# Performance work log

Measured on AMD Instinct MI355X. Metric: run time of the kernel, lower is better.

## Reference

```python
import jax, jax.numpy as jnp
import numpy as np
import math

B, S, D = 4, 4096, 2048
H = 16
DH = D // H  # 128
EPS = 1e-5


def _layer_norm(x, g, b):
    m = jnp.mean(x, axis=-1, keepdims=True)
    v = jnp.mean(jnp.square(x - m), axis=-1, keepdims=True)
    return (x - m) * jax.lax.rsqrt(v + EPS) * g + b


def setup_inputs() -> dict:
    key = jax.random.key(0)
    ks = jax.random.split(key, 12)
    s = 0.02
    return {
        "X": jax.random.normal(ks[0], (B, S, D), dtype=jnp.float32),
        "Wq": jax.random.normal(ks[1], (D, D), dtype=jnp.float32) * s,
        "bq": jnp.zeros((D,), dtype=jnp.float32),
        "Wk": jax.random.normal(ks[2], (D, D), dtype=jnp.float32) * s,
        "bk": jnp.zeros((D,), dtype=jnp.float32),
        "Wv": jax.random.normal(ks[3], (D, D), dtype=jnp.float32) * s,
        "bv": jnp.zeros((D,), dtype=jnp.float32),
        "g1": jnp.ones((D,), dtype=jnp.float32),
        "beta1": jnp.zeros((D,), dtype=jnp.float32),
        "W1": jax.random.normal(ks[4], (D, D), dtype=jnp.float32) * s,
        "b1": jnp.zeros((D,), dtype=jnp.float32),
        "W2": jax.random.normal(ks[5], (D, D), dtype=jnp.float32) * s,
        "b2": jnp.zeros((D,), dtype=jnp.float32),
        "g2": jnp.ones((D,), dtype=jnp.float32),
        "beta2": jnp.zeros((D,), dtype=jnp.float32),
    }


def reference(X, Wq, bq, Wk, bk, Wv, bv, g1, beta1, W1, b1, W2, b2, g2, beta2):
    # --- MultiHeadSelfAttention (faithful: .view, so attention is over HEADS per token) ---
    q = (X @ Wq + bq).reshape(B, S, H, DH)
    k = (X @ Wk + bk).reshape(B, S, H, DH)
    v = (X @ Wv + bv).reshape(B, S, H, DH)
    # [B, S, H, H] scores: heads attend to heads within the same position
    att = jnp.einsum('bshd,bstd->bsht', q, k) / math.sqrt(DH)
    att = jax.nn.softmax(att, axis=-1)
    y = jnp.einsum('bsht,bstd->bshd', att, v).reshape(B, S, D)
    # --- residual + LN1 ---
    X1 = _layer_norm(X + y, g1, beta1)
    # --- FeedForward: D -> D -> D with exact GELU ---
    h = jax.nn.gelu(X1 @ W1 + b1, approximate=False)
    y2 = h @ W2 + b2
    # --- residual + LN2 ---
    return _layer_norm(X1 + y2, g2, beta2)
```

## Files before the change

### kernel.cpp

```cpp
#include <hip/hip_runtime.h>
#include <math.h>

#define DM 2048
#define NT 16384
#define KD 2048

typedef __bf16 bf16x8 __attribute__((ext_vector_type(8)));
typedef float  f32x4  __attribute__((ext_vector_type(4)));

__device__ __forceinline__ void gld_lds16(const void* g, void* l) {
  __builtin_amdgcn_global_load_lds(
      (const __attribute__((address_space(1))) unsigned int*)g,
      (__attribute__((address_space(3))) unsigned int*)l, 16, 0, 0);
}

__global__ __launch_bounds__(256) void k_cast(const float* __restrict__ x,
                                              __bf16* __restrict__ y) {
  const size_t i = ((size_t)blockIdx.x * 256 + threadIdx.x) * 8;
  const float4 a = *(const float4*)(x + i);
  const float4 b = *(const float4*)(x + i + 4);
  bf16x8 o;
  o[0]=(__bf16)a.x; o[1]=(__bf16)a.y; o[2]=(__bf16)a.z; o[3]=(__bf16)a.w;
  o[4]=(__bf16)b.x; o[5]=(__bf16)b.y; o[6]=(__bf16)b.z; o[7]=(__bf16)b.w;
  *(bf16x8*)(y + i) = o;
}

__global__ __launch_bounds__(256) void k_transpose(const float* __restrict__ W,
                                                   __bf16* __restrict__ Wt) {
  __shared__ float t[32][33];
  const int tx = threadIdx.x, ty = threadIdx.y;
  const int n  = blockIdx.x * 32 + tx;
  const int k0 = blockIdx.y * 32;
  #pragma unroll
  for (int j = 0; j < 32; j += 8) t[ty + j][tx] = W[(size_t)(k0 + ty + j) * DM + n];
  __syncthreads();
  const int kk = k0 + tx;
  const int n0 = blockIdx.x * 32;
  #pragma unroll
  for (int j = 0; j < 32; j += 8)
    Wt[(size_t)(n0 + ty + j) * KD + kk] = (__bf16)t[tx][ty + j];
}

__global__ __launch_bounds__(256) void k_bias3(const float* __restrict__ a,
                                               const float* __restrict__ b,
                                               const float* __restrict__ c,
                                               float* __restrict__ o) {
  const int i = blockIdx.x * 256 + threadIdx.x;
  o[i] = (i < 2048) ? a[i] : ((i < 4096) ? b[i - 2048] : c[i - 4096]);
}

__global__ __launch_bounds__(256, 2) void k_gemm(
    const __bf16* __restrict__ A, const __bf16* __restrict__ Bt,
    const float* __restrict__ bias, const int mode, const int ntile_n,
    const int NS,
    __bf16* __restrict__ outb, const float* __restrict__ resf,
    const __bf16* __restrict__ resb, float* __restrict__ outf) {
  __shared__ __bf16 As[128 * 64];
  __shared__ __bf16 Bs[128 * 64];
  const int tid  = threadIdx.x;
  const int wave = tid >> 6, lane = tid & 63;
  const int quad = lane >> 4, r16 = lane & 15;
  const int bid = blockIdx.x;
  const int m0 = (bid / ntile_n) * 128;
  const int n0 = (bid % ntile_n) * 128;
  const int wm = (wave >> 1) * 64, wn = (wave & 1) * 64;

  const int lrow = lane >> 3;
  const int gblk = (lane & 7) ^ lrow;
  const __bf16* Ap[4];
  const __bf16* Bp[4];
  __bf16* AsW[4];
  __bf16* BsW[4];
  #pragma unroll
  for (int i = 0; i < 4; i++) {
    const int sr = i * 32 + wave * 8 + lrow;
    Ap[i] = A  + (size_t)(m0 + sr) * KD + gblk * 8;
    Bp[i] = Bt + (size_t)(n0 + sr) * KD + gblk * 8;
    AsW[i] = &As[i * 2048 + wave * 512];
    BsW[i] = &Bs[i * 2048 + wave * 512];
  }

  f32x4 acc[4][4] = {};

  for (int k0 = 0; k0 < KD; k0 += 64) {
    #pragma unroll
    for (int i = 0; i < 4; i++) {
      gld_lds16(Ap[i] + k0, AsW[i]);
      gld_lds16(Bp[i] + k0, BsW[i]);
    }
    __syncthreads();
    #pragma unroll
    for (int ks = 0; ks < 2; ks++) {
      const int fb = ((ks * 4 + quad) ^ (r16 & 7)) * 8;
      bf16x8 af[4], bfr[4];
      #pragma unroll
      for (int mi = 0; mi < 4; mi++)
        af[mi] = *(const bf16x8*)&As[(wm + mi * 16 + r16) * 64 + fb];
      #pragma unroll
      for (int ni = 0; ni < 4; ni++)
        bfr[ni] = *(const bf16x8*)&Bs[(wn + ni * 16 + r16) * 64 + fb];
      #pragma unroll
      for (int mi = 0; mi < 4; mi++)
        #pragma unroll
        for (int ni = 0; ni < 4; ni++)
          acc[mi][ni] = __builtin_amdgcn_mfma_f32_16x16x32_bf16(af[mi], bfr[ni], acc[mi][ni], 0, 0, 0);
    }
    __syncthreads();
  }

  if (mode <= 1) {
    __bf16* eb = &As[wave * 2048];
    #pragma unroll
    for (int half = 0; half < 2; half++) {
      #pragma unroll
      for (int nj = 0; nj < 2; nj++) {
        const int ni = half * 2 + nj;
        const int gn = n0 + wn + ni * 16 + r16;
        const float bv = bias[gn];
        #pragma unroll
        for (int mi = 0; mi < 4; mi++) {
          #pragma unroll
          for (int r = 0; r < 4; r++) {
            float v = acc[mi][ni][r] + bv;
            if (mode == 1) v = 0.5f * v * (1.0f + erff(v * 0.70710678118654752f));
            eb[(mi * 16 + quad * 4 + r) * 32 + nj * 16 + r16] = (__bf16)v;
          }
        }
      }
      #pragma unroll
      for (int rd = 0; rd < 4; rd++) {
        const int row = rd * 16 + (lane >> 2);
        const int c0 = (lane & 3) * 8;
        bf16x8 vv = *(const bf16x8*)&eb[row * 32 + c0];
        *(bf16x8*)(outb + (size_t)(m0 + wm + row) * NS + n0 + wn + half * 32 + c0) = vv;
      }
    }
  } else {
    #pragma unroll
    for (int ni = 0; ni < 4; ni++) {
      const int gn = n0 + wn + ni * 16 + r16;
      const float bv = bias[gn];
      #pragma unroll
      for (int mi = 0; mi < 4; mi++) {
        const int gm = m0 + wm + mi * 16 + quad * 4;
        if (mode == 2) {
          #pragma unroll
          for (int r = 0; r < 4; r++) {
            const size_t o = (size_t)(gm + r) * NS + gn;
            outf[o] = acc[mi][ni][r] + bv + resf[o];
          }
        } else {
          #pragma unroll
          for (int r = 0; r < 4; r++) {
            const size_t o = (size_t)(gm + r) * NS + gn;
            outf[o] = acc[mi][ni][r] + bv + (float)resb[o];
          }
        }
      }
    }
  }
}

__global__ __launch_bounds__(256) void k_attn_ln1(
    const __bf16* __restrict__ QKV, const float* __restrict__ X,
    const float* __restrict__ g1, const float* __restrict__ be1,
    float* __restrict__ X1, __bf16* __restrict__ X1b, const int use_f32) {
  __shared__ float qs[16 * 132];
  __shared__ float ks[16 * 132];
  __shared__ float vs[16 * 132];
  __shared__ float p[256];
  __shared__ float red[8];
  const int tid = threadIdx.x;
  const size_t qbase = (size_t)blockIdx.x * 6144;
  const size_t base  = (size_t)blockIdx.x * DM;
  const int e0 = tid * 8;

  {
    const int row = e0 >> 7, c0 = e0 & 127;
    bf16x8 qv = *(const bf16x8*)(QKV + qbase + e0);
    bf16x8 kv = *(const bf16x8*)(QKV + qbase + 2048 + e0);
    bf16x8 vv = *(const bf16x8*)(QKV + qbase + 4096 + e0);
    #pragma unroll
    for (int j = 0; j < 8; j++) {
      qs[row * 132 + c0 + j] = (float)qv[j];
      ks[row * 132 + c0 + j] = (float)kv[j];
      vs[row * 132 + c0 + j] = (float)vv[j];
    }
  }
  __syncthreads();

  {
    const int h = tid >> 4, t = tid & 15;
    const float* qp = &qs[h * 132];
    const float* kp = &ks[t * 132];
    float s = 0.f;
    #pragma unroll
    for (int d = 0; d < 128; d++) s += qp[d] * kp[d];
    s *= 0.08838834764831845f;
    float mx = s;
    #pragma unroll
    for (int off = 8; off; off >>= 1) mx = fmaxf(mx, __shfl_xor(mx, off, 16));
    const float e = expf(s - mx);
    float sum = e;
    #pragma unroll
    for (int off = 8; off; off >>= 1) sum += __shfl_xor(sum, off, 16);
    p[tid] = e / sum;
  }
  __syncthreads();

  float zloc[8];
  float zs = 0.f, zq = 0.f;
  {
    const float4 x1 = *(const float4*)(X + base + e0);
    const float4 x2 = *(const float4*)(X + base + e0 + 4);
    const float xr[8] = {x1.x, x1.y, x1.z, x1.w, x2.x, x2.y, x2.z, x2.w};
    const int hh = e0 >> 7;
    const int d0 = e0 & 127;
    const float* pp = &p[hh * 16];
    #pragma unroll
    for (int j = 0; j < 8; j++) {
      float y = 0.f;
      #pragma unroll
      for (int t2 = 0; t2 < 16; t2++) y += pp[t2] * vs[t2 * 132 + d0 + j];
      const float z = xr[j] + y;
      zloc[j] = z; zs += z; zq += z * z;
    }
  }
  #pragma unroll
  for (int off = 32; off; off >>= 1) {
    zs += __shfl_xor(zs, off, 64);
    zq += __shfl_xor(zq, off, 64);
  }
  const int wave = tid >> 6, lane = tid & 63;
  if (lane == 0) { red[wave] = zs; red[4 + wave] = zq; }
  __syncthreads();
  zs = red[0] + red[1] + red[2] + red[3];
  zq = red[4] + red[5] + red[6] + red[7];
  const float mean = zs * (1.f / DM);
  const float var = zq * (1.f / DM) - mean * mean;
  const float rstd = rsqrtf(var + 1e-5f);
  {
    float o[8];
    #pragma unroll
    for (int j = 0; j < 8; j++)
      o[j] = (zloc[j] - mean) * rstd * g1[e0 + j] + be1[e0 + j];
    if (use_f32) {
      *(float4*)(X1 + base + e0)     = make_float4(o[0], o[1], o[2], o[3]);
      *(float4*)(X1 + base + e0 + 4) = make_float4(o[4], o[5], o[6], o[7]);
    }
    bf16x8 ob;
    #pragma unroll
    for (int j = 0; j < 8; j++) ob[j] = (__bf16)o[j];
    *(bf16x8*)(X1b + base + e0) = ob;
  }
}

__global__ __launch_bounds__(256) void k_ln2(const float* __restrict__ Z,
                                             const float* __restrict__ g,
                                             const float* __restrict__ be,
                                             float* __restrict__ out) {
  __shared__ float red[8];
  const int tid = threadIdx.x;
  const size_t base = (size_t)blockIdx.x * DM;
  const int e0 = tid * 8;
  const float4 a = *(const float4*)(Z + base + e0);
  const float4 b = *(const float4*)(Z + base + e0 + 4);
  float z[8] = {a.x, a.y, a.z, a.w, b.x, b.y, b.z, b.w};
  float zs = 0.f, zq = 0.f;
  #pragma unroll
  for (int j = 0; j < 8; j++) { zs += z[j]; zq += z[j] * z[j]; }
  #pragma unroll
  for (int off = 32; off; off >>= 1) {
    zs += __shfl_xor(zs, off, 64);
    zq += __shfl_xor(zq, off, 64);
  }
  const int wave = tid >> 6, lane = tid & 63;
  if (lane == 0) { red[wave] = zs; red[4 + wave] = zq; }
  __syncthreads();
  zs = red[0] + red[1] + red[2] + red[3];
  zq = red[4] + red[5] + red[6] + red[7];
  const float mean = zs * (1.f / DM);
  const float var = zq * (1.f / DM) - mean * mean;
  const float rstd = rsqrtf(var + 1e-5f);
  float o[8];
  #pragma unroll
  for (int j = 0; j < 8; j++)
    o[j] = (z[j] - mean) * rstd * g[e0 + j] + be[e0 + j];
  *(float4*)(out + base + e0)     = make_float4(o[0], o[1], o[2], o[3]);
  *(float4*)(out + base + e0 + 4) = make_float4(o[4], o[5], o[6], o[7]);
}

extern "C" void kernel_launch(void* const* d_in, const int* in_sizes, int n_in,
                              void* d_out, int out_size, void* d_ws, size_t ws_size,
                              hipStream_t stream) {
  const float* X   = (const float*)d_in[0];
  const float* Wq  = (const float*)d_in[1];
  const float* bq  = (const float*)d_in[2];
  const float* Wk  = (const float*)d_in[3];
  const float* bk  = (const float*)d_in[4];
  const float* Wv  = (const float*)d_in[5];
  const float* bv  = (const float*)d_in[6];
  const float* g1  = (const float*)d_in[7];
  const float* be1 = (const float*)d_in[8];
  const float* W1  = (const float*)d_in[9];
  const float* b1  = (const float*)d_in[10];
  const float* W2  = (const float*)d_in[11];
  const float* b2  = (const float*)d_in[12];
  const float* g2  = (const float*)d_in[13];
  const float* be2 = (const float*)d_in[14];
  float* out = (float*)d_out;

  char* ws = (char*)d_ws;
  size_t off = 0;
  auto alloc = [&](size_t b) -> char* {
    char* p = ws + off;
    off += (b + 255) & ~(size_t)255;
    return p;
  };
  const size_t EL  = (size_t)NT * DM;
  const size_t EL3 = (size_t)NT * 6144;
  __bf16* Xb    = (__bf16*)alloc(EL * 2);
  __bf16* Wqkvt = (__bf16*)alloc((size_t)6144 * KD * 2);
  __bf16* W1t   = (__bf16*)alloc((size_t)DM * KD * 2);
  __bf16* W2t   = (__bf16*)alloc((size_t)DM * KD * 2);
  float*  b3    = (float*)alloc(6144 * 4);
  __bf16* QKVb  = (__bf16*)alloc(EL3 * 2);
  __bf16* X1b   = (__bf16*)alloc(EL * 2);
  const int use_f32 = (ws_size >= off + EL * 4) ? 1 : 0;
  float* X1 = nullptr;
  if (use_f32) X1 = (float*)alloc(EL * 4);
  __bf16* Hb = Xb;
  float*  Z  = (float*)QKVb;

  k_cast<<<dim3(NT * DM / 2048), dim3(256), 0, stream>>>(X, Xb);
  dim3 tb(32, 8), tg(64, 64);
  k_transpose<<<tg, tb, 0, stream>>>(Wq, Wqkvt);
  k_transpose<<<tg, tb, 0, stream>>>(Wk, Wqkvt + (size_t)2048 * KD);
  k_transpose<<<tg, tb, 0, stream>>>(Wv, Wqkvt + (size_t)4096 * KD);
  k_transpose<<<tg, tb, 0, stream>>>(W1, W1t);
  k_transpose<<<tg, tb, 0, stream>>>(W2, W2t);
  k_bias3<<<dim3(24), dim3(256), 0, stream>>>(bq, bk, bv, b3);

  k_gemm<<<dim3((NT / 128) * 48), dim3(256), 0, stream>>>(
      Xb, Wqkvt, b3, 0, 48, 6144, QKVb, nullptr, nullptr, nullptr);
  k_attn_ln1<<<dim3(NT), dim3(256), 0, stream>>>(QKVb, X, g1, be1, X1, X1b, use_f32);
  k_gemm<<<dim3((NT / 128) * 16), dim3(256), 0, stream>>>(
      X1b, W1t, b1, 1, 16, 2048, Hb, nullptr, nullptr, nullptr);
  k_gemm<<<dim3((NT / 128) * 16), dim3(256), 0, stream>>>(
      Hb, W2t, b2, use_f32 ? 2 : 3, 16, 2048, nullptr, X1, X1b, Z);
  k_ln2<<<dim3(NT), dim3(256), 0, stream>>>(Z, g2, be2, out);
}
```

Baseline: 1.240 ms.

## Pipeline GEMM K-loop with 4-stage LDS ring buffer and tile swizzle

Replaces the single-buffered 64-wide K loop, which synchronized twice per step, with a 4-stage ring of 32-wide K slices. Loads are issued three stages ahead using direct global-to-LDS copies, and a partial vmcnt wait with one barrier per step lets memory traffic overlap the MFMA work. It also remaps block IDs in groups of 8 for better L2 locality and raises wave priority around the MFMA block. The cost is 64KB of LDS, which limits occupancy, and the code now assumes KD=2048 with a hardcoded iteration count and no LDS swizzle, so bank conflicts may appear.

After: 1.405 ms. 1.13x slower.

```diff
diff --git a/kernel.cpp b/kernel.cpp
--- a/kernel.cpp
+++ b/kernel.cpp
@@ -55,61 +55,77 @@
     const int NS,
     __bf16* __restrict__ outb, const float* __restrict__ resf,
     const __bf16* __restrict__ resb, float* __restrict__ outf) {
-  __shared__ __bf16 As[128 * 64];
-  __shared__ __bf16 Bs[128 * 64];
+  __shared__ __bf16 lds[4 * 8192];
   const int tid  = threadIdx.x;
-  const int wave = tid >> 6, lane = tid & 63;
+  const int w = tid >> 6, lane = tid & 63;
   const int quad = lane >> 4, r16 = lane & 15;
-  const int bid = blockIdx.x;
-  const int m0 = (bid / ntile_n) * 128;
-  const int n0 = (bid % ntile_n) * 128;
-  const int wm = (wave >> 1) * 64, wn = (wave & 1) * 64;
-
-  const int lrow = lane >> 3;
-  const int gblk = (lane & 7) ^ lrow;
-  const __bf16* Ap[4];
-  const __bf16* Bp[4];
-  __bf16* AsW[4];
-  __bf16* BsW[4];
-  #pragma unroll
-  for (int i = 0; i < 4; i++) {
-    const int sr = i * 32 + wave * 8 + lrow;
-    Ap[i] = A  + (size_t)(m0 + sr) * KD + gblk * 8;
-    Bp[i] = Bt + (size_t)(n0 + sr) * KD + gblk * 8;
-    AsW[i] = &As[i * 2048 + wave * 512];
-    BsW[i] = &Bs[i * 2048 + wave * 512];
-  }
+  const int wm = (w >> 1) * 64, wn = (w & 1) * 64;
+
+  const int nwg = gridDim.x;
+  const int sw  = (blockIdx.x & 7) * (nwg >> 3) + (blockIdx.x >> 3);
+  const int m0 = (sw / ntile_n) * 128;
+  const int n0 = (sw % ntile_n) * 128;
+
+  const int srow = (w << 5) + (lane >> 2);
+  const __bf16* aSrc = A  + (size_t)(m0 + srow) * KD + (lane & 3) * 8;
+  const __bf16* bSrc = Bt + (size_t)(n0 + srow) * KD + (lane & 3) * 8;
+
+  const int aoff = (wm + r16) * 32 + quad * 8;
+  const int boff = 4096 + (wn + r16) * 32 + quad * 8;
 
   f32x4 acc[4][4] = {};
 
-  for (int k0 = 0; k0 < KD; k0 += 64) {
-    #pragma unroll
-    for (int i = 0; i < 4; i++) {
-      gld_lds16(Ap[i] + k0, AsW[i]);
-      gld_lds16(Bp[i] + k0, BsW[i]);
-    }
-    __syncthreads();
-    #pragma unroll
-    for (int ks = 0; ks < 2; ks++) {
-      const int fb = ((ks * 4 + quad) ^ (r16 & 7)) * 8;
-      bf16x8 af[4], bfr[4];
-      #pragma unroll
-      for (int mi = 0; mi < 4; mi++)
-        af[mi] = *(const bf16x8*)&As[(wm + mi * 16 + r16) * 64 + fb];
-      #pragma unroll
-      for (int ni = 0; ni < 4; ni++)
-        bfr[ni] = *(const bf16x8*)&Bs[(wn + ni * 16 + r16) * 64 + fb];
-      #pragma unroll
-      for (int mi = 0; mi < 4; mi++)
-        #pragma unroll
-        for (int ni = 0; ni < 4; ni++)
-          acc[mi][ni] = __builtin_amdgcn_mfma_f32_16x16x32_bf16(af[mi], bfr[ni], acc[mi][ni], 0, 0, 0);
-    }
-    __syncthreads();
-  }
+#define STAGE(q) { \
+    const int so = ((q) & 3) * 8192; \
+    gld_lds16(aSrc + (q) * 32,                   lds + so + (w << 10)); \
+    gld_lds16(aSrc + (size_t)16 * KD + (q) * 32, lds + so + (w << 10) + 512); \
+    gld_lds16(bSrc + (q) * 32,                   lds + so + 4096 + (w << 10)); \
+    gld_lds16(bSrc + (size_t)16 * KD + (q) * 32, lds + so + 4096 + (w << 10) + 512); \
+  }
+
+#define COMPUTE(s) { \
+    const int so = ((s) & 3) * 8192; \
+    bf16x8 af[4], bfr[4]; \
+    _Pragma("unroll") \
+    for (int mi = 0; mi < 4; ++mi) af[mi] = *(const bf16x8*)&lds[so + aoff + mi * 512]; \
+    _Pragma("unroll") \
+    for (int ni = 0; ni < 4; ++ni) bfr[ni] = *(const bf16x8*)&lds[so + boff + ni * 512]; \
+    __builtin_amdgcn_s_setprio(1); \
+    _Pragma("unroll") \
+    for (int mi = 0; mi < 4; ++mi) { \
+      _Pragma("unroll") \
+      for (int ni = 0; ni < 4; ++ni) \
+        acc[mi][ni] = __builtin_amdgcn_mfma_f32_16x16x32_bf16(af[mi], bfr[ni], acc[mi][ni], 0, 0, 0); \
+    } \
+    __builtin_amdgcn_s_setprio(0); \
+  }
+
+#define WAITBAR(n) { \
+    asm volatile("s_waitcnt vmcnt(" #n ")" ::: "memory"); \
+    __builtin_amdgcn_s_barrier(); \
+    asm volatile("" ::: "memory"); \
+  }
+
+  STAGE(0) STAGE(1) STAGE(2)
+  WAITBAR(8)
+
+  for (int s = 0; s < 60; ++s) {
+    STAGE(s + 3)
+    COMPUTE(s)
+    WAITBAR(8)
+  }
+  STAGE(63) COMPUTE(60) WAITBAR(8)
+  COMPUTE(61) WAITBAR(4)
+  COMPUTE(62) WAITBAR(0)
+  COMPUTE(63)
+  __syncthreads();
+
+#undef STAGE
+#undef COMPUTE
+#undef WAITBAR
 
   if (mode <= 1) {
-    __bf16* eb = &As[wave * 2048];
+    __bf16* eb = &lds[w * 2048];
     #pragma unroll
     for (int half = 0; half < 2; half++) {
       #pragma unroll
```
